# Performance work log

Measured on AMD Instinct MI355X. Metric: run time of the kernel, lower is better.

Reference implementation:

```python
import jax, jax.numpy as jnp
import numpy as np

N, P, S, M, K, L = 1024, 4, 12, 64, 16, 8
SNR = 20.0
PWR = 1.0
DECAY = L // 2  # Channel is built with decay = L // 2
MK = M + K
SMK = (S + 1) * MK
LOUT = L + SMK - 1  # full linear-convolution length


def _to_c(x):
    return x[..., 0] + 1j * x[..., 1]


def _to_r(x):
    return jnp.stack([x.real, x.imag], axis=-1)


def setup_inputs() -> dict:
    key = jax.random.key(0)
    k1, k2, k3, k4 = jax.random.split(key, 4)
    return {
        "x": jax.random.normal(k1, (N, P, S, M, 2), jnp.float32),
        "pilot_raw": jax.random.normal(k2, (N, P, 1, M, 2), jnp.float32),
        "cof_unit": jax.random.normal(k3, (N, P, L, 2), jnp.float32),
        "noise_unit": jax.random.normal(k4, (N, P, S + 1, MK, 2), jnp.float32),
    }


def reference(x, pilot_raw, cof_unit, noise_unit):
    # --- pilot: Normalize -> ifft -> add CP (done once in torch __init__) ---
    power = jnp.mean(pilot_raw ** 2, axis=(-2, -1), keepdims=True)  # (N,P,1,1,1)
    alpha = jnp.sqrt(PWR / 2) / jnp.sqrt(power)
    pilot = jnp.fft.ifft(_to_c(alpha * pilot_raw), axis=-1)          # (N,P,1,M) complex
    pilot = jnp.concatenate([pilot[..., -K:], pilot], axis=-1)        # add CP -> (N,P,1,MK)

    # --- payload: ifft -> add CP ---
    xt = jnp.fft.ifft(_to_c(x), axis=-1)                              # (N,P,S,M)
    xt = jnp.concatenate([xt[..., -K:], xt], axis=-1)                 # (N,P,S,MK)

    sig = jnp.concatenate([pilot, xt], axis=2).reshape(N, P, SMK)     # serialized complex signal

    # --- channel taps: sqrt(power_profile/2) * randn (cof is None path) ---
    prof = jnp.exp(-jnp.arange(L, dtype=jnp.float32) / DECAY)
    prof = prof / jnp.sum(prof)
    cof = _to_c(jnp.sqrt(prof / 2)[:, None] * cof_unit)               # (N,P,L) complex

    cof_true = jnp.concatenate([cof, jnp.zeros((N, P, M - L), cof.dtype)], axis=-1)
    H_true = jnp.fft.fft(cof_true, axis=-1)                           # (N,P,M)

    # --- L-tap linear convolution (equivalent to dense Toeplitz bmm) ---
    s_pad = jnp.pad(sig, ((0, 0), (0, 0), (L - 1, L - 1)))            # (N,P,SMK+2(L-1))
    y = jnp.zeros((N, P, LOUT), sig.dtype)
    for t in range(L):  # fixed small tap count
        y = y + cof[:, :, t:t + 1] * s_pad[:, :, L - 1 - t: L - 1 - t + LOUT]

    out = y[:, :, :SMK].reshape(N, P, S + 1, MK)

    # --- AWGN (default SNR path, isTest=False) ---
    noise_pwr = PWR / (M * 10.0 ** (0.1 * SNR))
    out = out + np.sqrt(noise_pwr / 2) * _to_c(noise_unit)

    # --- split pilot/signal, remove CP, FFT back to frequency domain ---
    info_pilot = jnp.fft.fft(out[:, :, 0:1, K:], axis=-1)             # (N,P,1,M)
    info_sig = jnp.fft.fft(out[:, :, 1:, K:], axis=-1)                # (N,P,S,M)

    return (_to_r(info_pilot), _to_r(info_sig), _to_r(H_true),
            jnp.float32(noise_pwr))
```

## Files before the change

kernel.cpp:

```cpp
#include <hip/hip_runtime.h>
#include <math.h>

#define NN   1024
#define PP   4
#define SS   12
#define MM   64
#define KK   16
#define LL   8
#define MKK  80
#define NSYM 13

#define OFF_PILOT  0
#define OFF_SIG    524288
#define OFF_H      6815744
#define OFF_SCALAR 7340032

#define NOISE_PWR   1.5625e-4f
#define NOISE_SCALE 8.8388347648318447e-3f
#define INV_2SUM    0.1279105570f


__device__ __forceinline__ float2 shflx(float2 v, int mask) {
    return make_float2(__shfl_xor(v.x, mask), __shfl_xor(v.y, mask));
}
__device__ __forceinline__ float2 cmul(float2 a, float2 b) {
    return make_float2(a.x*b.x - a.y*b.y, a.x*b.y + a.y*b.x);
}

template<int NS>
__device__ __forceinline__ void fft64_dit(float2* v, const float2* tw, const float* sgn) {
    #pragma unroll
    for (int s = 0; s < 6; ++s) {
        const float sg = sgn[s], tx = tw[s].x, ty = tw[s].y;
        float ax[NS], ay[NS];
        #pragma unroll
        for (int j = 0; j < NS; ++j) {
            ax[j] = v[j].x * tx - v[j].y * ty;
            ay[j] = v[j].x * ty + v[j].y * tx;
        }
        float2 o[NS];
        #pragma unroll
        for (int j = 0; j < NS; ++j) o[j] = shflx(make_float2(ax[j], ay[j]), 1 << s);
        #pragma unroll
        for (int j = 0; j < NS; ++j) {
            v[j].x = fmaf(sg, ax[j], o[j].x);
            v[j].y = fmaf(sg, ay[j], o[j].y);
        }
    }
}

__global__ __launch_bounds__(256) void ofdm_kernel(
    const float2* __restrict__ x,
    const float2* __restrict__ pilot_raw,
    const float2* __restrict__ cof_unit,
    const float2* __restrict__ noise_unit,
    float2* __restrict__ out_pilot,
    float2* __restrict__ out_sig,
    float2* __restrict__ out_H,
    float*  __restrict__ out_scalar)
{
    const int b    = blockIdx.x;
    const int tid  = threadIdx.x;
    const int wid  = tid >> 6;
    const int lane = tid & 63;

    const float2* xb = x          + (size_t)b * (SS*MM);
    const float2* pb = pilot_raw  + (size_t)b * MM;
    const float2* cb = cof_unit   + (size_t)b * LL;
    const float2* nb = noise_unit + (size_t)b * (NSYM*MKK);

    const int rb = (int)(__brev((unsigned)lane) >> 26);

    float2 cof[LL];
    #pragma unroll
    for (int t = 0; t < LL; ++t) {
        float2 u = cb[t];
        float sc = sqrtf(__expf(-(float)t * 0.25f) * INV_2SUM);
        cof[t] = make_float2(sc * u.x, sc * u.y);
    }

    float2 tw[6];
    float  sgn[6];
    #pragma unroll
    for (int s = 0; s < 6; ++s) {
        const int h = 1 << s;
        const bool up = (lane & h) != 0;
        sgn[s] = up ? -1.0f : 1.0f;
        float ang = -6.2831853071795864769f * (float)(lane & (h - 1)) / (float)(2 * h);
        float sn, cs;
        __sincosf(ang, &sn, &cs);
        tw[s] = up ? make_float2(cs, sn) : make_float2(1.0f, 0.0f);
    }

    float sn, cs;
    __sincosf(-0.0981747704246810387f * (float)lane, &sn, &cs);
    const float2 w = make_float2(cs, sn);
    float2 H = cof[LL - 1];
    #pragma unroll
    for (int l = LL - 2; l >= 0; --l) {
        float2 Hw = cmul(H, w);
        H = make_float2(Hw.x + cof[l].x, Hw.y + cof[l].y);
    }

    const size_t ob  = (size_t)b * MM;
    const size_t osb = (size_t)b * (SS * MM);

    if (wid == 1) out_H[ob + lane] = H;

    if (wid == 0) {
        float2 nv[4];
        nv[0] = nb[ 0*MKK + KK + rb];
        nv[1] = nb[ 4*MKK + KK + rb];
        nv[2] = nb[ 8*MKK + KK + rb];
        nv[3] = nb[12*MKK + KK + rb];
        float2 pv = pb[lane];
        float2 X1 = xb[ 3*MM + lane];
        float2 X2 = xb[ 7*MM + lane];
        float2 X3 = xb[11*MM + lane];
        #pragma unroll
        for (int j = 0; j < 4; ++j) {
            nv[j].x *= NOISE_SCALE; nv[j].y *= NOISE_SCALE;
        }
        fft64_dit<4>(nv, tw, sgn);

        float ssq = pv.x * pv.x + pv.y * pv.y;
        #pragma unroll
        for (int off = 32; off > 0; off >>= 1)
            ssq += __shfl_xor(ssq, off);
        float alpha = sqrtf(64.0f / ssq);
        float2 X0 = make_float2(alpha * pv.x, alpha * pv.y);

        float2 o0 = cmul(H, X0), o1 = cmul(H, X1), o2 = cmul(H, X2), o3 = cmul(H, X3);
        out_pilot[ob + lane]          = make_float2(o0.x + nv[0].x, o0.y + nv[0].y);
        out_sig[osb +  3*MM + lane]   = make_float2(o1.x + nv[1].x, o1.y + nv[1].y);
        out_sig[osb +  7*MM + lane]   = make_float2(o2.x + nv[2].x, o2.y + nv[2].y);
        out_sig[osb + 11*MM + lane]   = make_float2(o3.x + nv[3].x, o3.y + nv[3].y);
    } else {
        float2 nv[3];
        nv[0] = nb[(wid    ) * MKK + KK + rb];
        nv[1] = nb[(wid + 4) * MKK + KK + rb];
        nv[2] = nb[(wid + 8) * MKK + KK + rb];
        float2 X0 = xb[(wid - 1) * MM + lane];
        float2 X1 = xb[(wid + 3) * MM + lane];
        float2 X2 = xb[(wid + 7) * MM + lane];
        #pragma unroll
        for (int j = 0; j < 3; ++j) {
            nv[j].x *= NOISE_SCALE; nv[j].y *= NOISE_SCALE;
        }
        fft64_dit<3>(nv, tw, sgn);

        float2 o0 = cmul(H, X0), o1 = cmul(H, X1), o2 = cmul(H, X2);
        out_sig[osb + (wid - 1) * MM + lane] = make_float2(o0.x + nv[0].x, o0.y + nv[0].y);
        out_sig[osb + (wid + 3) * MM + lane] = make_float2(o1.x + nv[1].x, o1.y + nv[1].y);
        out_sig[osb + (wid + 7) * MM + lane] = make_float2(o2.x + nv[2].x, o2.y + nv[2].y);
    }

    if (b == 0 && tid == 0) out_scalar[0] = NOISE_PWR;
}

extern "C" void kernel_launch(void* const* d_in, const int* in_sizes, int n_in,
                              void* d_out, int out_size, void* d_ws, size_t ws_size,
                              hipStream_t stream) {
    const float2* x  = (const float2*)d_in[0];
    const float2* pr = (const float2*)d_in[1];
    const float2* cu = (const float2*)d_in[2];
    const float2* nu = (const float2*)d_in[3];

    float* out = (float*)d_out;
    float2* out_pilot = (float2*)(out + OFF_PILOT);
    float2* out_sig   = (float2*)(out + OFF_SIG);
    float2* out_H     = (float2*)(out + OFF_H);
    float*  out_sc    = out + OFF_SCALAR;

    ofdm_kernel<<<dim3(NN*PP), dim3(256), 0, stream>>>(
        x, pr, cu, nu, out_pilot, out_sig, out_H, out_sc);
}
```

Before: 106.1 us.

## Split 64-point FFT into paired 32-point half-wave FFTs with float4 noise loads

Restructures the per-symbol 64-point FFT: each half-wave runs a 32-point shuffle FFT on even and odd samples loaded together as float4, followed by one final radix-2 stage with a w64 twiddle. Symbols are redistributed so each wave processes pairs of symbols, one per half-wave. This is meant to cut shuffle stages and memory transactions by vectorizing noise and coefficient loads. In exchange it adds H shuffles and divergent branches, and one half-wave is left idle on the odd final symbol.

```diff
diff --git a/kernel.cpp b/kernel.cpp
--- a/kernel.cpp
+++ b/kernel.cpp
@@ -18,6 +18,7 @@
 #define NOISE_PWR   1.5625e-4f
 #define NOISE_SCALE 8.8388347648318447e-3f
 #define INV_2SUM    0.1279105570f
+#define W64_ANG    -0.09817477042468103f
 
 
 __device__ __forceinline__ float2 shflx(float2 v, int mask) {
@@ -27,26 +28,23 @@
     return make_float2(a.x*b.x - a.y*b.y, a.x*b.y + a.y*b.x);
 }
 
-template<int NS>
-__device__ __forceinline__ void fft64_dit(float2* v, const float2* tw, const float* sgn) {
+__device__ __forceinline__ void fft64_pair(float2& vE, float2& vO,
+                                           const float2* tw5, const float* sgn5,
+                                           float2 w32) {
     #pragma unroll
-    for (int s = 0; s < 6; ++s) {
-        const float sg = sgn[s], tx = tw[s].x, ty = tw[s].y;
-        float ax[NS], ay[NS];
-        #pragma unroll
-        for (int j = 0; j < NS; ++j) {
-            ax[j] = v[j].x * tx - v[j].y * ty;
-            ay[j] = v[j].x * ty + v[j].y * tx;
-        }
-        float2 o[NS];
-        #pragma unroll
-        for (int j = 0; j < NS; ++j) o[j] = shflx(make_float2(ax[j], ay[j]), 1 << s);
-        #pragma unroll
-        for (int j = 0; j < NS; ++j) {
-            v[j].x = fmaf(sg, ax[j], o[j].x);
-            v[j].y = fmaf(sg, ay[j], o[j].y);
-        }
+    for (int s = 0; s < 5; ++s) {
+        const float tx = tw5[s].x, ty = tw5[s].y, sg = sgn5[s];
+        float2 aE = make_float2(vE.x*tx - vE.y*ty, vE.x*ty + vE.y*tx);
+        float2 aO = make_float2(vO.x*tx - vO.y*ty, vO.x*ty + vO.y*tx);
+        float2 oE = shflx(aE, 1 << s);
+        float2 oO = shflx(aO, 1 << s);
+        vE = make_float2(fmaf(sg, aE.x, oE.x), fmaf(sg, aE.y, oE.y));
+        vO = make_float2(fmaf(sg, aO.x, oO.x), fmaf(sg, aO.y, oO.y));
     }
+    float2 aO = cmul(vO, w32);
+    const float ex = vE.x, ey = vE.y;
+    vE = make_float2(ex + aO.x, ey + aO.y);
+    vO = make_float2(ex - aO.x, ey - aO.y);
 }
 
 __global__ __launch_bounds__(256) void ofdm_kernel(
@@ -63,97 +61,94 @@
     const int tid  = threadIdx.x;
     const int wid  = tid >> 6;
     const int lane = tid & 63;
+    const int l5   = lane & 31;
+    const int half = lane >> 5;
+    const int rb5  = (int)(__brev((unsigned)l5) >> 27);
 
-    const float2* xb = x          + (size_t)b * (SS*MM);
-    const float2* pb = pilot_raw  + (size_t)b * MM;
-    const float2* cb = cof_unit   + (size_t)b * LL;
-    const float2* nb = noise_unit + (size_t)b * (NSYM*MKK);
+    const float2* xb  = x          + (size_t)b * (SS*MM);
+    const float2* pb  = pilot_raw  + (size_t)b * MM;
+    const float4* cb4 = (const float4*)(cof_unit + (size_t)b * LL);
+    const float4* nb4 = (const float4*)(noise_unit + (size_t)b * (NSYM*MKK));
 
-    const int rb = (int)(__brev((unsigned)lane) >> 26);
-
-    float2 cof[LL];
+    float4 cq0 = cb4[0], cq1 = cb4[1], cq2 = cb4[2], cq3 = cb4[3];
+    float2 cof[LL] = {
+        {cq0.x, cq0.y}, {cq0.z, cq0.w}, {cq1.x, cq1.y}, {cq1.z, cq1.w},
+        {cq2.x, cq2.y}, {cq2.z, cq2.w}, {cq3.x, cq3.y}, {cq3.z, cq3.w}};
     #pragma unroll
     for (int t = 0; t < LL; ++t) {
-        float2 u = cb[t];
         float sc = sqrtf(__expf(-(float)t * 0.25f) * INV_2SUM);
-        cof[t] = make_float2(sc * u.x, sc * u.y);
+        cof[t].x *= sc; cof[t].y *= sc;
     }
 
-    float2 tw[6];
-    float  sgn[6];
-    #pragma unroll
-    for (int s = 0; s < 6; ++s) {
-        const int h = 1 << s;
-        const bool up = (lane & h) != 0;
-        sgn[s] = up ? -1.0f : 1.0f;
-        float ang = -6.2831853071795864769f * (float)(lane & (h - 1)) / (float)(2 * h);
-        float sn, cs;
-        __sincosf(ang, &sn, &cs);
-        tw[s] = up ? make_float2(cs, sn) : make_float2(1.0f, 0.0f);
-    }
-
-    float sn, cs;
-    __sincosf(-0.0981747704246810387f * (float)lane, &sn, &cs);
-    const float2 w = make_float2(cs, sn);
+    float sH, cH;
+    __sincosf(W64_ANG * (float)lane, &sH, &cH);
+    const float2 wH = make_float2(cH, sH);
     float2 H = cof[LL - 1];
     #pragma unroll
     for (int l = LL - 2; l >= 0; --l) {
-        float2 Hw = cmul(H, w);
+        float2 Hw = cmul(H, wH);
         H = make_float2(Hw.x + cof[l].x, Hw.y + cof[l].y);
     }
+
+    float2 tw5[5];
+    float  sgn5[5];
+    #pragma unroll
+    for (int s = 0; s < 5; ++s) {
+        const int h = 1 << s;
+        const bool up = (l5 & h) != 0;
+        sgn5[s] = up ? -1.0f : 1.0f;
+        float ang = -3.14159265358979323846f * (float)(l5 & (h - 1)) / (float)h;
+        float sn, cs;
+        __sincosf(ang, &sn, &cs);
+        tw5[s] = up ? make_float2(cs, sn) : make_float2(1.0f, 0.0f);
+    }
+    float sW, cW;
+    __sincosf(W64_ANG * (float)l5, &sW, &cW);
+    const float2 w32 = make_float2(cW, sW);
 
     const size_t ob  = (size_t)b * MM;
     const size_t osb = (size_t)b * (SS * MM);
 
-    if (wid == 1) out_H[ob + lane] = H;
+    auto do_pair = [&](int symA, int symB, bool storeB) {
+        const int sym = half ? symB : symA;
+        float4 nq = nb4[sym * (MKK/2) + (KK/2) + rb5];
+        float2 vE = make_float2(NOISE_SCALE * nq.x, NOISE_SCALE * nq.y);
+        float2 vO = make_float2(NOISE_SCALE * nq.z, NOISE_SCALE * nq.w);
+        float2 HE = make_float2(__shfl(H.x, l5),      __shfl(H.y, l5));
+        float2 HO = make_float2(__shfl(H.x, l5 | 32), __shfl(H.y, l5 | 32));
+        float2 X1, X2;
+        if (sym == 0) {
+            float2 p1 = pb[l5], p2 = pb[l5 + 32];
+            float ssq = p1.x*p1.x + p1.y*p1.y + p2.x*p2.x + p2.y*p2.y;
+            #pragma unroll
+            for (int off = 16; off > 0; off >>= 1)
+                ssq += __shfl_xor(ssq, off);
+            float alpha = sqrtf(64.0f / ssq);
+            X1 = make_float2(alpha * p1.x, alpha * p1.y);
+            X2 = make_float2(alpha * p2.x, alpha * p2.y);
+        } else {
+            X1 = xb[(sym - 1) * MM + l5];
+            X2 = xb[(sym - 1) * MM + l5 + 32];
+        }
+        fft64_pair(vE, vO, tw5, sgn5, w32);
+        float2 r1 = cmul(HE, X1); r1.x += vE.x; r1.y += vE.y;
+        float2 r2 = cmul(HO, X2); r2.x += vO.x; r2.y += vO.y;
+        if (half == 0 || storeB) {
+            if (sym == 0) {
+                out_pilot[ob + l5]      = r1;
+                out_pilot[ob + l5 + 32] = r2;
+            } else {
+                float2* o = out_sig + osb + (size_t)(sym - 1) * MM;
+                o[l5]      = r1;
+                o[l5 + 32] = r2;
+            }
+        }
+    };
 
-    if (wid == 0) {
-        float2 nv[4];
-        nv[0] = nb[ 0*MKK + KK + rb];
-        nv[1] = nb[ 4*MKK + KK + rb];
-        nv[2] = nb[ 8*MKK + KK + rb];
-        nv[3] = nb[12*MKK + KK + rb];
-        float2 pv = pb[lane];
-        float2 X1 = xb[ 3*MM + lane];
-        float2 X2 = xb[ 7*MM + lane];
-        float2 X3 = xb[11*MM + lane];
-        #pragma unroll
-        for (int j = 0; j < 4; ++j) {
-            nv[j].x *= NOISE_SCALE; nv[j].y *= NOISE_SCALE;
-        }
-        fft64_dit<4>(nv, tw, sgn);
-
-        float ssq = pv.x * pv.x + pv.y * pv.y;
-        #pragma unroll
-        for (int off = 32; off > 0; off >>= 1)
-            ssq += __shfl_xor(ssq, off);
-        float alpha = sqrtf(64.0f / ssq);
-        float2 X0 = make_float2(alpha * pv.x, alpha * pv.y);
-
-        float2 o0 = cmul(H, X0), o1 = cmul(H, X1), o2 = cmul(H, X2), o3 = cmul(H, X3);
-        out_pilot[ob + lane]          = make_float2(o0.x + nv[0].x, o0.y + nv[0].y);
-        out_sig[osb +  3*MM + lane]   = make_float2(o1.x + nv[1].x, o1.y + nv[1].y);
-        out_sig[osb +  7*MM + lane]   = make_float2(o2.x + nv[2].x, o2.y + nv[2].y);
-        out_sig[osb + 11*MM + lane]   = make_float2(o3.x + nv[3].x, o3.y + nv[3].y);
-    } else {
-        float2 nv[3];
-        nv[0] = nb[(wid    ) * MKK + KK + rb];
-        nv[1] = nb[(wid + 4) * MKK + KK + rb];
-        nv[2] = nb[(wid + 8) * MKK + KK + rb];
-        float2 X0 = xb[(wid - 1) * MM + lane];
-        float2 X1 = xb[(wid + 3) * MM + lane];
-        float2 X2 = xb[(wid + 7) * MM + lane];
-        #pragma unroll
-        for (int j = 0; j < 3; ++j) {
-            nv[j].x *= NOISE_SCALE; nv[j].y *= NOISE_SCALE;
-        }
-        fft64_dit<3>(nv, tw, sgn);
-
-        float2 o0 = cmul(H, X0), o1 = cmul(H, X1), o2 = cmul(H, X2);
-        out_sig[osb + (wid - 1) * MM + lane] = make_float2(o0.x + nv[0].x, o0.y + nv[0].y);
-        out_sig[osb + (wid + 3) * MM + lane] = make_float2(o1.x + nv[1].x, o1.y + nv[1].y);
-        out_sig[osb + (wid + 7) * MM + lane] = make_float2(o2.x + nv[2].x, o2.y + nv[2].y);
-    }
+    if      (wid == 0) { do_pair(0, 1, true);  do_pair(8, 9, true);   }
+    else if (wid == 1) { do_pair(2, 3, true);  do_pair(10, 11, true); }
+    else if (wid == 2) { do_pair(4, 5, true);  do_pair(12, 12, false); }
+    else               { do_pair(6, 7, true);  out_H[ob + lane] = H;  }
 
     if (b == 0 && tid == 0) out_scalar[0] = NOISE_PWR;
 }
```

New measurement: 106.9 us. Within noise of the previous version (+0.7%).
